# Kernel tuning notes

Measured on AMD Instinct MI355X. Metric: run time of the kernel, lower is better.

The kernel has to match this reference:

```python
import jax, jax.numpy as jnp
import numpy as np

F = 10000   # n_features
H = 64      # hidden_size
NC = 2      # n_class


def setup_inputs() -> dict:
    key = jax.random.key(0)
    ks = jax.random.split(key, 16)
    he_lstm = np.float32(np.sqrt(2.0 / (H + 1)))
    he_1 = np.float32(np.sqrt(2.0))
    return {
        "tim": 100,
        "X": jax.random.normal(ks[0], (F,), jnp.float32),
        "X_hap": jax.random.normal(ks[1], (F,), jnp.float32),
        "mask": jax.random.randint(ks[2], (F,), 0, 2, jnp.int32),
        "last_occured": jax.random.randint(ks[3], (F,), 0, 100, jnp.int32),
        "Ht": jax.random.normal(ks[4], (F, H), jnp.float32),
        "Ct": jnp.zeros((F, H), jnp.float32),
        "c_t": jnp.zeros((H,), jnp.float32),
        "lstm_weights": he_lstm * jax.random.normal(ks[5], (F, 4 * H, H + 1), jnp.float32),
        "lstm_bias": jnp.zeros((F, 4 * H), jnp.float32),
        "lstm_xT_weights": he_1 * jax.random.normal(ks[6], (F, H), jnp.float32),
        "lstm_xT_bias": jnp.zeros((F, H), jnp.float32),
        "lstm_delT_weights": he_1 * jax.random.normal(ks[7], (F, 2 * H), jnp.float32),
        "lstm_c_inp_weights": jax.random.normal(ks[8], (F, H), jnp.float32),
        "lstm_cf_weights": jax.random.normal(ks[9], (F, H), jnp.float32),
        "lstm_c_out_weights": jax.random.normal(ks[10], (F, H), jnp.float32),
        "mlp_w1": jax.random.normal(ks[11], (2 * H, 2 * H), jnp.float32) / np.float32(np.sqrt(2 * H)),
        "mlp_b1": jnp.zeros((2 * H,), jnp.float32),
        "mlp_w2": jax.random.normal(ks[12], (NC, 2 * H), jnp.float32) / np.float32(np.sqrt(2 * H)),
        "mlp_b2": jnp.zeros((NC,), jnp.float32),
    }


def reference(tim, X, X_hap, mask, last_occured, Ht, Ct, c_t,
              lstm_weights, lstm_bias, lstm_xT_weights, lstm_xT_bias,
              lstm_delT_weights, lstm_c_inp_weights, lstm_cf_weights,
              lstm_c_out_weights, mlp_w1, mlp_b1, mlp_w2, mlp_b2):
    # masked (dense-equivalent) form of the per-feature gather/scatter cell.
    m = mask == 1                                   # [F] bool
    mf = m.astype(jnp.float32)[:, None]             # [F,1]
    delta = jnp.float32(tim) - last_occured.astype(jnp.float32)  # [F]

    # cur_input = [x_f, h_f] -> gates via per-feature matmul [F,4H,H+1] @ [F,H+1]
    cur_input = jnp.concatenate([X[:, None], Ht], axis=-1)        # [F,H+1]
    gates = jnp.einsum('fgh,fh->fg', lstm_weights, cur_input) + lstm_bias  # [F,4H]

    xm_T = lstm_xT_weights * X[:, None] + lstm_xT_bias            # [F,H]
    del_T = lstm_delT_weights * delta[:, None]                    # [F,2H] (no bias, as original)

    gi_pre, gf_pre, go_pre, pre_c = jnp.split(gates, 4, axis=-1)  # each [F,H]
    gi = jax.nn.sigmoid(gi_pre + lstm_c_inp_weights * c_t)
    gf = jax.nn.sigmoid(gf_pre + lstm_cf_weights * c_t)
    del_Tt, del_To = jnp.split(del_T, 2, axis=-1)
    T_t = jax.nn.sigmoid(xm_T + del_Tt)
    pre_c = jnp.tanh(pre_c)

    agg_c = gf * c_t + gi * T_t * pre_c                           # [F,H]
    go = jax.nn.sigmoid(go_pre + lstm_c_out_weights * agg_c + del_To)
    h_new = go * jnp.tanh(agg_c)                                  # [F,H]

    cnt = jnp.maximum(mf.sum(), 1.0)
    C_curr = (mf * agg_c).sum(axis=0) / cnt                       # mean over observed feats [H]
    H_curr = jnp.where(m.any(), mf * h_new, Ht)                   # scatter into zeros, fallback Ht
    H_mean = (mf * H_curr).sum(axis=0) / cnt                      # mean over current feats [H]

    inp = jnp.concatenate([C_curr, H_mean])                       # [2H]
    logits = mlp_w2 @ jax.nn.relu(mlp_w1 @ inp + mlp_b1) + mlp_b2
    pred = jax.nn.softmax(logits, axis=0)
    return pred, H_curr, C_curr
```

## Files before the change

kernel.cpp:

```cpp
#include <hip/hip_runtime.h>
#include <math.h>

#define FN 10000
#define HN 64
#define GN 256
#define KX 65

__device__ __forceinline__ float sigmoidf_(float x) {
    return 1.0f / (1.0f + __expf(-x));
}

__global__ __launch_bounds__(1024) void k_init(const int* __restrict__ mask,
                                               const void* __restrict__ tim_raw,
                                               float* __restrict__ ws, int n) {
    __shared__ int red[16];
    int tid = threadIdx.x;
    int s = 0;
    for (int i = tid; i < n; i += 1024) s += (mask[i] == 1) ? 1 : 0;
    for (int off = 32; off; off >>= 1) s += __shfl_down(s, off);
    int wave = tid >> 6;
    if ((tid & 63) == 0) red[wave] = s;
    __syncthreads();
    if (tid < 128) ws[tid] = 0.0f;
    if (tid == 0) {
        int tot = 0;
        for (int w = 0; w < 16; ++w) tot += red[w];
        ws[128] = (float)tot;
        ws[129] = (tot > 0) ? 1.0f : 0.0f;
        int ti = *(const int*)tim_raw;
        float tf;
        if (ti >= 0 && ti < (1 << 20)) tf = (float)ti;
        else tf = *(const float*)tim_raw;
        ws[130] = tf;
    }
}

__global__ __launch_bounds__(256) void lstm_main(
    const float* __restrict__ X, const int* __restrict__ mask,
    const int* __restrict__ last_occ, const float* __restrict__ Ht,
    const float* __restrict__ c_t,
    const float* __restrict__ W,
    const float* __restrict__ Wb,
    const float* __restrict__ xT_w, const float* __restrict__ xT_b,
    const float* __restrict__ delT_w,
    const float* __restrict__ c_inp_w, const float* __restrict__ cf_w,
    const float* __restrict__ c_out_w,
    float* __restrict__ ws,
    float* __restrict__ out)
{
    __shared__ float xs[72];
    __shared__ float4 wt4[1040];
    __shared__ float gs[GN];
    float* wt = (float*)wt4;

    const int f   = blockIdx.x;
    const int tid = threadIdx.x;

    if (tid < KX) xs[tid] = (tid == 0) ? X[f] : Ht[(size_t)f * HN + (tid - 1)];

    const float* Wf = W + (size_t)f * (GN * KX);
    const int g = tid >> 2;
    const int p = tid & 3;

    for (int c = 0; c < 4; ++c) {
        const float4* src = (const float4*)(Wf + c * (64 * KX));
        for (int i = tid; i < 1040; i += 256) wt4[i] = src[i];
        __syncthreads();

        const float* wrow = wt + g * KX + p * 16;
        const float* xp   = xs + p * 16;
        float acc = 0.0f;
        #pragma unroll
        for (int j = 0; j < 16; ++j) acc += wrow[j] * xp[j];
        if (p == 3) acc += wt[g * KX + 64] * xs[64];
        acc += __shfl_xor(acc, 1);
        acc += __shfl_xor(acc, 2);
        if (p == 0) gs[c * 64 + g] = acc + Wb[(size_t)f * GN + c * 64 + g];
        __syncthreads();
    }

    if (tid < HN) {
        const int h = tid;
        const size_t fh = (size_t)f * HN + h;
        const float anyf  = ws[129];
        const float timf  = ws[130];
        const float delta = timf - (float)last_occ[f];
        const float ct    = c_t[h];
        const float Xf    = xs[0];

        float gi     = sigmoidf_(gs[h]        + c_inp_w[fh] * ct);
        float gf     = sigmoidf_(gs[64 + h]   + cf_w[fh] * ct);
        float go_pre = gs[128 + h];
        float prec   = tanhf(gs[192 + h]);
        float xmT    = xT_w[fh] * Xf + xT_b[fh];
        float dTt    = delT_w[(size_t)f * 2 * HN + h] * delta;
        float dTo    = delT_w[(size_t)f * 2 * HN + HN + h] * delta;
        float Tt     = sigmoidf_(xmT + dTt);
        float aggc   = gf * ct + gi * Tt * prec;
        float go     = sigmoidf_(go_pre + c_out_w[fh] * aggc + dTo);
        float hnew   = go * tanhf(aggc);

        const bool  msk = (mask[f] == 1);
        const float mf  = msk ? 1.0f : 0.0f;
        out[2 + fh] = (anyf > 0.5f) ? (mf * hnew) : xs[h + 1];
        if (msk) {
            atomicAdd(&ws[h], aggc);
            atomicAdd(&ws[64 + h], hnew);
        }
    }
}

__global__ __launch_bounds__(256) void k_final(
    const float* __restrict__ ws,
    const float* __restrict__ w1, const float* __restrict__ b1,
    const float* __restrict__ w2, const float* __restrict__ b2,
    float* __restrict__ out)
{
    __shared__ float inp[128];
    __shared__ float hid[128];
    const int tid = threadIdx.x;
    const float cnt = fmaxf(ws[128], 1.0f);
    if (tid < 128) inp[tid] = ws[tid] / cnt;
    if (tid < 64)  out[2 + FN * HN + tid] = ws[tid] / cnt;
    __syncthreads();

    const int i = tid >> 1, half = tid & 1;
    const float* wrow = w1 + i * 128 + half * 64;
    const float* ip   = inp + half * 64;
    float pacc = 0.0f;
    #pragma unroll
    for (int j = 0; j < 64; ++j) pacc += wrow[j] * ip[j];
    pacc += __shfl_xor(pacc, 1);
    if (half == 0) hid[i] = fmaxf(pacc + b1[i], 0.0f);
    __syncthreads();

    if (tid < 64) {
        float p0 = 0.0f, p1 = 0.0f;
        for (int j = tid; j < 128; j += 64) {
            p0 += w2[j] * hid[j];
            p1 += w2[128 + j] * hid[j];
        }
        for (int off = 32; off; off >>= 1) {
            p0 += __shfl_down(p0, off);
            p1 += __shfl_down(p1, off);
        }
        if (tid == 0) {
            float l0 = p0 + b2[0], l1 = p1 + b2[1];
            float m  = fmaxf(l0, l1);
            float e0 = __expf(l0 - m), e1 = __expf(l1 - m);
            out[0] = e0 / (e0 + e1);
            out[1] = e1 / (e0 + e1);
        }
    }
}

extern "C" void kernel_launch(void* const* d_in, const int* in_sizes, int n_in,
                              void* d_out, int out_size, void* d_ws, size_t ws_size,
                              hipStream_t stream) {
    const void*  tim_raw = d_in[0];
    const float* X       = (const float*)d_in[1];
    const int*   mask    = (const int*)d_in[3];
    const int*   last_oc = (const int*)d_in[4];
    const float* Ht      = (const float*)d_in[5];
    const float* c_t     = (const float*)d_in[7];
    const float* W       = (const float*)d_in[8];
    const float* Wb      = (const float*)d_in[9];
    const float* xT_w    = (const float*)d_in[10];
    const float* xT_b    = (const float*)d_in[11];
    const float* delT_w  = (const float*)d_in[12];
    const float* ci_w    = (const float*)d_in[13];
    const float* cf_w    = (const float*)d_in[14];
    const float* co_w    = (const float*)d_in[15];
    const float* w1      = (const float*)d_in[16];
    const float* b1      = (const float*)d_in[17];
    const float* w2      = (const float*)d_in[18];
    const float* b2      = (const float*)d_in[19];

    float* out = (float*)d_out;
    float* ws  = (float*)d_ws;

    k_init<<<1, 1024, 0, stream>>>(mask, tim_raw, ws, FN);
    lstm_main<<<FN, 256, 0, stream>>>(X, mask, last_oc, Ht, c_t, W, Wb,
                                      xT_w, xT_b, delT_w, ci_w, cf_w, co_w,
                                      ws, out);
    k_final<<<1, 256, 0, stream>>>(ws, w1, b1, w2, b2, out);
}
```

Measured before the change: 930.2 us.

## Double-buffer LSTM weight chunks via direct global-to-LDS loads, per-wave

Each wave now streams its own 16-row slice of every gate chunk straight into LDS using global_load_lds. It double-buffers across the four chunks, with explicit vmcnt waits instead of block-wide __syncthreads. Inputs are kept in registers, and each p==0 thread holds all four gate pre-activations for one hidden unit, so the shared gate buffer and the serialized load-sync-compute loop go away. The aim is to overlap weight streaming with the dot products and to raise achieved bandwidth on this memory-bound kernel. The cost is more LDS per block and hand-written waitcnt encodings, which rely on in-order vmcnt accounting.

```diff
diff --git a/kernel.cpp b/kernel.cpp
--- a/kernel.cpp
+++ b/kernel.cpp
@@ -5,6 +5,13 @@
 #define HN 64
 #define GN 256
 #define KX 65
+
+typedef const __attribute__((address_space(1))) void* gas1_t;
+typedef __attribute__((address_space(3))) void* las3_t;
+
+__device__ __forceinline__ void lds_load16(const void* g, void* l) {
+    __builtin_amdgcn_global_load_lds((gas1_t)g, (las3_t)l, 16, 0, 0);
+}
 
 __device__ __forceinline__ float sigmoidf_(float x) {
     return 1.0f / (1.0f + __expf(-x));
@@ -45,64 +52,98 @@
     const float* __restrict__ delT_w,
     const float* __restrict__ c_inp_w, const float* __restrict__ cf_w,
     const float* __restrict__ c_out_w,
+    const float* __restrict__ ws_in,
     float* __restrict__ ws,
     float* __restrict__ out)
 {
-    __shared__ float xs[72];
-    __shared__ float4 wt4[1040];
-    __shared__ float gs[GN];
-    float* wt = (float*)wt4;
-
-    const int f   = blockIdx.x;
-    const int tid = threadIdx.x;
-
-    if (tid < KX) xs[tid] = (tid == 0) ? X[f] : Ht[(size_t)f * HN + (tid - 1)];
-
-    const float* Wf = W + (size_t)f * (GN * KX);
-    const int g = tid >> 2;
-    const int p = tid & 3;
-
+    __shared__ float wbuf[2][4160];
+
+    const int f    = blockIdx.x;
+    const int tid  = threadIdx.x;
+    const int w    = tid >> 6;
+    const int lane = tid & 63;
+    const int q    = lane >> 2;
+    const int p    = tid & 3;
+    const int hq   = w * 16 + q;
+
+    float xr[16];
+    {
+        const float* HtF = Ht + (size_t)f * HN;
+        #pragma unroll
+        for (int j = 0; j < 16; ++j) {
+            int idx = p * 16 + j;
+            xr[j] = (idx == 0) ? X[f] : HtF[idx - 1];
+        }
+    }
+    const float x64 = Ht[(size_t)f * HN + 63];
+
+    const float4* Wf4 = (const float4*)(W + (size_t)f * (GN * KX));
+
+    {
+        const float4* src = Wf4 + w * 260;
+        float* dst = &wbuf[0][w * 1040];
+        #pragma unroll
+        for (int k = 0; k < 4; ++k)
+            lds_load16(src + k * 64 + lane, dst + k * 256);
+        if (lane < 4) lds_load16(src + 256 + lane, dst + 1024);
+    }
+
+    float ga[4];
+    #pragma unroll
     for (int c = 0; c < 4; ++c) {
-        const float4* src = (const float4*)(Wf + c * (64 * KX));
-        for (int i = tid; i < 1040; i += 256) wt4[i] = src[i];
-        __syncthreads();
-
-        const float* wrow = wt + g * KX + p * 16;
-        const float* xp   = xs + p * 16;
+        if (c < 3) {
+            const float4* src = Wf4 + (c + 1) * 1040 + w * 260;
+            float* dst = &wbuf[(c + 1) & 1][w * 1040];
+            #pragma unroll
+            for (int k = 0; k < 4; ++k)
+                lds_load16(src + k * 64 + lane, dst + k * 256);
+            if (lane < 4) lds_load16(src + 256 + lane, dst + 1024);
+            __builtin_amdgcn_sched_barrier(0);
+            __builtin_amdgcn_s_waitcnt(0x0F75);
+            __builtin_amdgcn_sched_barrier(0);
+        } else {
+            __builtin_amdgcn_sched_barrier(0);
+            __builtin_amdgcn_s_waitcnt(0x0F70);
+            __builtin_amdgcn_sched_barrier(0);
+        }
+
+        const float* row = &wbuf[c & 1][w * 1040 + q * 65 + p * 16];
         float acc = 0.0f;
         #pragma unroll
-        for (int j = 0; j < 16; ++j) acc += wrow[j] * xp[j];
-        if (p == 3) acc += wt[g * KX + 64] * xs[64];
+        for (int j = 0; j < 16; ++j) acc += row[j] * xr[j];
+        if (p == 3) acc += wbuf[c & 1][w * 1040 + q * 65 + 64] * x64;
         acc += __shfl_xor(acc, 1);
         acc += __shfl_xor(acc, 2);
-        if (p == 0) gs[c * 64 + g] = acc + Wb[(size_t)f * GN + c * 64 + g];
-        __syncthreads();
-    }
-
-    if (tid < HN) {
-        const int h = tid;
+        ga[c] = acc;
+    }
+
+    if (p == 0) {
+        const int h = hq;
         const size_t fh = (size_t)f * HN + h;
-        const float anyf  = ws[129];
-        const float timf  = ws[130];
+        const size_t fg = (size_t)f * GN;
+        const float b0 = Wb[fg + h];
+        const float b1 = Wb[fg + 64 + h];
+        const float b2 = Wb[fg + 128 + h];
+        const float b3 = Wb[fg + 192 + h];
+        const float anyf = ws_in[129];
+        const float timf = ws_in[130];
         const float delta = timf - (float)last_occ[f];
-        const float ct    = c_t[h];
-        const float Xf    = xs[0];
-
-        float gi     = sigmoidf_(gs[h]        + c_inp_w[fh] * ct);
-        float gf     = sigmoidf_(gs[64 + h]   + cf_w[fh] * ct);
-        float go_pre = gs[128 + h];
-        float prec   = tanhf(gs[192 + h]);
-        float xmT    = xT_w[fh] * Xf + xT_b[fh];
-        float dTt    = delT_w[(size_t)f * 2 * HN + h] * delta;
-        float dTo    = delT_w[(size_t)f * 2 * HN + HN + h] * delta;
-        float Tt     = sigmoidf_(xmT + dTt);
-        float aggc   = gf * ct + gi * Tt * prec;
-        float go     = sigmoidf_(go_pre + c_out_w[fh] * aggc + dTo);
-        float hnew   = go * tanhf(aggc);
-
-        const bool  msk = (mask[f] == 1);
-        const float mf  = msk ? 1.0f : 0.0f;
-        out[2 + fh] = (anyf > 0.5f) ? (mf * hnew) : xs[h + 1];
+        const float ct = c_t[h];
+        const float Xf = xr[0];
+
+        float gi   = sigmoidf_(ga[0] + b0 + c_inp_w[fh] * ct);
+        float gf   = sigmoidf_(ga[1] + b1 + cf_w[fh] * ct);
+        float prec = tanhf(ga[3] + b3);
+        float xmT  = xT_w[fh] * Xf + xT_b[fh];
+        float dTt  = delT_w[(size_t)f * 2 * HN + h] * delta;
+        float dTo  = delT_w[(size_t)f * 2 * HN + HN + h] * delta;
+        float Tt   = sigmoidf_(xmT + dTt);
+        float aggc = gf * ct + gi * Tt * prec;
+        float go   = sigmoidf_(ga[2] + b2 + c_out_w[fh] * aggc + dTo);
+        float hnew = go * tanhf(aggc);
+
+        const bool msk = (mask[f] == 1);
+        out[2 + fh] = (anyf > 0.5f) ? (msk ? hnew : 0.0f) : Ht[fh];
         if (msk) {
             atomicAdd(&ws[h], aggc);
             atomicAdd(&ws[64 + h], hnew);
@@ -182,6 +223,6 @@
     k_init<<<1, 1024, 0, stream>>>(mask, tim_raw, ws, FN);
     lstm_main<<<FN, 256, 0, stream>>>(X, mask, last_oc, Ht, c_t, W, Wb,
                                       xT_w, xT_b, delT_w, ci_w, cf_w, co_w,
-                                      ws, out);
+                                      ws, ws, out);
     k_final<<<1, 256, 0, stream>>>(ws, w1, b1, w2, b2, out);
 }
```

Measured after the change: 898.8 us. 1.03x faster.
